# Kernel optimization log

Measured on AMD Instinct MI355X. Metric: run time of the kernel, lower is better.

Reference implementation:

```python
import jax, jax.numpy as jnp
import numpy as np
import math

HIDDEN = 2048
N_HEADS = 8
N_KV_HEADS = 1
HEAD_DIM = 256
ROPE_THETA = 10000.0
B, S = 1, 4096


def setup_inputs() -> dict:
    key = jax.random.key(0)
    ks = jax.random.split(key, 5)
    hidden_states = jax.random.normal(ks[0], (B, S, HIDDEN), dtype=jnp.float32)
    attention_mask = jnp.zeros((B, 1, S, S), dtype=jnp.float32)
    position_ids = jnp.arange(S, dtype=jnp.int64 if jax.config.jax_enable_x64 else jnp.int32)[None, :].repeat(B, axis=0)
    scale = 1.0 / math.sqrt(HIDDEN)
    Wq = jax.random.normal(ks[1], (HIDDEN, N_HEADS * HEAD_DIM), dtype=jnp.float32) * scale
    Wk = jax.random.normal(ks[2], (HIDDEN, N_KV_HEADS * HEAD_DIM), dtype=jnp.float32) * scale
    Wv = jax.random.normal(ks[3], (HIDDEN, N_KV_HEADS * HEAD_DIM), dtype=jnp.float32) * scale
    Wo = jax.random.normal(ks[4], (N_HEADS * HEAD_DIM, HIDDEN), dtype=jnp.float32) * scale
    return {"hidden_states": hidden_states, "attention_mask": attention_mask,
            "position_ids": position_ids, "Wq": Wq, "Wk": Wk, "Wv": Wv, "Wo": Wo}


def _rope_cos_sin(position_ids):
    # inv_freq: [HEAD_DIM/2]
    inv_freq = 1.0 / (ROPE_THETA ** (jnp.arange(0, HEAD_DIM, 2, dtype=jnp.float32) / HEAD_DIM))
    freqs = position_ids.astype(jnp.float32)[:, :, None] * inv_freq[None, None, :]  # [b,s,d/2]
    emb = jnp.concatenate([freqs, freqs], axis=-1)  # [b,s,d]
    return jnp.cos(emb), jnp.sin(emb)


def _rotate_half(x):
    x1, x2 = jnp.split(x, 2, axis=-1)
    return jnp.concatenate([-x2, x1], axis=-1)


def reference(hidden_states, attention_mask, position_ids, Wq, Wk, Wv, Wo):
    b, s, _ = hidden_states.shape
    g = N_HEADS // N_KV_HEADS  # kv groups
    # projections -> [b, heads, s, d]
    q = (hidden_states @ Wq).reshape(b, s, N_HEADS, HEAD_DIM).transpose(0, 2, 1, 3)
    k = (hidden_states @ Wk).reshape(b, s, N_KV_HEADS, HEAD_DIM).transpose(0, 2, 1, 3)
    v = (hidden_states @ Wv).reshape(b, s, N_KV_HEADS, HEAD_DIM).transpose(0, 2, 1, 3)
    # rotary embedding
    cos, sin = _rope_cos_sin(position_ids)  # [b,s,d]
    cos = cos[:, None, :, :]
    sin = sin[:, None, :, :]
    q = q * cos + _rotate_half(q) * sin
    k = k * cos + _rotate_half(k) * sin
    # GQA: group q heads against shared kv heads (no materialized repeat_kv)
    qg = q.reshape(b, N_KV_HEADS, g, s, HEAD_DIM)
    scores = jnp.einsum('bkgqd,bkld->bkgql', qg, k) / math.sqrt(HEAD_DIM)  # [b,kv,g,s,s]
    scores = scores.reshape(b, N_HEADS, s, s) + attention_mask
    attn = jax.nn.softmax(scores, axis=-1)
    out = jnp.einsum('bkgql,bkld->bkgqd', attn.reshape(b, N_KV_HEADS, g, s, s), v)
    out = out.reshape(b, N_HEADS, s, HEAD_DIM).transpose(0, 2, 1, 3).reshape(b, s, N_HEADS * HEAD_DIM)
    return out @ Wo
```

## Files before the change

kernel.cpp:

```cpp
#include <hip/hip_runtime.h>

typedef __bf16 bf16x8 __attribute__((ext_vector_type(8)));
typedef float f32x4 __attribute__((ext_vector_type(4)));
typedef float f32x16 __attribute__((ext_vector_type(16)));
typedef unsigned int u32x4 __attribute__((ext_vector_type(4)));
typedef unsigned short u16x4 __attribute__((ext_vector_type(4)));

__device__ __forceinline__ unsigned short f2bf(float f) {
  unsigned int u = __float_as_uint(f);
  u += 0x7FFF + ((u >> 16) & 1);
  return (unsigned short)(u >> 16);
}
__device__ __forceinline__ unsigned int packbf(float a, float b) {
  return (unsigned int)f2bf(a) | ((unsigned int)f2bf(b) << 16);
}
__device__ __forceinline__ void gl2lds16(const void* g, void* l) {
  __builtin_amdgcn_global_load_lds(
      (const __attribute__((address_space(1))) unsigned int*)(unsigned long long)g,
      (__attribute__((address_space(3))) unsigned int*)(unsigned long long)l,
      16, 0, 0);
}

__global__ void cvt_bf16_kernel(const float* __restrict__ in,
                                unsigned short* __restrict__ out, int n) {
  int i = (blockIdx.x * 256 + threadIdx.x) * 4;
  if (i >= n) return;
  float4 v = *(const float4*)&in[i];
  u16x4 o = { f2bf(v.x), f2bf(v.y), f2bf(v.z), f2bf(v.w) };
  *(u16x4*)&out[i] = o;
}

__global__ void transpose_cvt_kernel(const float* __restrict__ in,
                                     unsigned short* __restrict__ out, int R, int C) {
  __shared__ float t[32][33];
  int c0 = blockIdx.x * 32, r0 = blockIdx.y * 32;
  int tx = threadIdx.x & 31, ty = threadIdx.x >> 5;
#pragma unroll
  for (int i = 0; i < 4; i++)
    t[ty + i * 8][tx] = in[(size_t)(r0 + ty + i * 8) * C + c0 + tx];
  __syncthreads();
#pragma unroll
  for (int i = 0; i < 4; i++)
    out[(size_t)(c0 + ty + i * 8) * R + r0 + tx] = f2bf(t[tx][ty + i * 8]);
}

__global__ void rope_kernel(const float* __restrict__ Qf, const float* __restrict__ Kf,
                            const int* __restrict__ pos_ids,
                            unsigned short* __restrict__ Qb, unsigned short* __restrict__ Kimg) {
  int i = blockIdx.x * 256 + threadIdx.x;
  const int QN = 4096 * 1024;
  int s, d;
  float x1, x2;
  int h = 0;
  bool isQ = (i < QN);
  if (isQ) {
    s = i >> 10;
    int rem = i & 1023;
    h = rem >> 7;
    d = rem & 127;
    size_t b = (size_t)s * 2048 + h * 256 + d;
    x1 = Qf[b];
    x2 = Qf[b + 128];
  } else {
    int j = i - QN;
    if (j >= 4096 * 128) return;
    s = j >> 7;
    d = j & 127;
    x1 = Kf[(size_t)s * 256 + d];
    x2 = Kf[(size_t)s * 256 + d + 128];
  }
  int p = pos_ids[s];
  float invf = (float)exp2(-(double)d * (13.287712379549449 / 128.0));
  float th = (float)p * invf;
  double thd = (double)th;
  float c = (float)cos(thd), sn = (float)sin(thd);
  float o1 = x1 * c - x2 * sn;
  float o2 = x2 * c + x1 * sn;
  if (isQ) {
    size_t base = ((size_t)h * 4096 + s) * 256;
    Qb[base + d] = f2bf(o1 * 0.0625f);
    Qb[base + d + 128] = f2bf(o2 * 0.0625f);
  } else {
    int blk = s >> 5, kk = s & 31;
    size_t base = (size_t)blk * 8192 + kk * 256;
    int d1 = d, d2 = d + 128;
    Kimg[base + (((d1 >> 3) ^ (kk & 15)) * 8) + (d1 & 7)] = f2bf(o1);
    Kimg[base + (((d2 >> 3) ^ (kk & 15)) * 8) + (d2 & 7)] = f2bf(o2);
  }
}

__global__ void vimg_kernel(const float* __restrict__ Vf, unsigned short* __restrict__ Vimg) {
  __shared__ float t[32][257];
  int blk = blockIdx.x;
  int tid = threadIdx.x;
#pragma unroll
  for (int i = 0; i < 32; i++)
    t[i][tid] = Vf[((size_t)blk * 32 + i) * 256 + tid];
  __syncthreads();
  int d = tid;
  unsigned short* out = Vimg + (size_t)blk * 8192 + d * 32;
#pragma unroll
  for (int c = 0; c < 4; c++) {
    u16x4 a = { f2bf(t[c*8+0][d]), f2bf(t[c*8+1][d]), f2bf(t[c*8+2][d]), f2bf(t[c*8+3][d]) };
    u16x4 b = { f2bf(t[c*8+4][d]), f2bf(t[c*8+5][d]), f2bf(t[c*8+6][d]), f2bf(t[c*8+7][d]) };
    int cc = ((c ^ (d & 3)) * 8);
    *(u16x4*)&out[cc] = a;
    *(u16x4*)&out[cc + 4] = b;
  }
}

__global__ __launch_bounds__(256) void gemm_bt_kernel(
    const unsigned short* __restrict__ A, const unsigned short* __restrict__ BT,
    float* __restrict__ C0, float* __restrict__ C1, float* __restrict__ C2,
    int K, int mode) {
  __shared__ unsigned short As[128 * 32];
  __shared__ unsigned short Bs[128 * 32];
  int tid = threadIdx.x;
  int lane = tid & 63, w = tid >> 6;
  int quad = lane >> 4, l16 = lane & 15;
  int wr = w >> 1, wc = w & 1;
  int m0 = blockIdx.x * 128, n0 = blockIdx.y * 128;
  f32x4 acc[4][4] = {};

  for (int k0 = 0; k0 < K; k0 += 32) {
#pragma unroll
    for (int i = 0; i < 2; i++) {
      int idx = tid + i * 256;
      int row = idx >> 2, c = idx & 3;
      int sw = (c ^ (row & 3) ^ ((row >> 2) & 3)) * 8;
      *(u32x4*)&As[row * 32 + sw] = *(const u32x4*)&A[(size_t)(m0 + row) * K + k0 + c * 8];
      *(u32x4*)&Bs[row * 32 + sw] = *(const u32x4*)&BT[(size_t)(n0 + row) * K + k0 + c * 8];
    }
    __syncthreads();
    bf16x8 af[4], bfr[4];
#pragma unroll
    for (int mt = 0; mt < 4; mt++) {
      int r = wr * 64 + mt * 16 + l16;
      af[mt] = *(const bf16x8*)&As[r * 32 + ((quad ^ (r & 3) ^ ((r >> 2) & 3)) * 8)];
    }
#pragma unroll
    for (int nt = 0; nt < 4; nt++) {
      int r = wc * 64 + nt * 16 + l16;
      bfr[nt] = *(const bf16x8*)&Bs[r * 32 + ((quad ^ (r & 3) ^ ((r >> 2) & 3)) * 8)];
    }
#pragma unroll
    for (int mt = 0; mt < 4; mt++)
#pragma unroll
      for (int nt = 0; nt < 4; nt++)
        acc[mt][nt] = __builtin_amdgcn_mfma_f32_16x16x32_bf16(af[mt], bfr[nt], acc[mt][nt], 0, 0, 0);
    __syncthreads();
  }

  float* Cb;
  int ld, coff;
  if (mode == 0 || n0 < 2048) { Cb = C0; ld = 2048; coff = 0; }
  else if (n0 < 2304)         { Cb = C1; ld = 256;  coff = 2048; }
  else                        { Cb = C2; ld = 256;  coff = 2304; }
#pragma unroll
  for (int mt = 0; mt < 4; mt++) {
    int row = m0 + wr * 64 + mt * 16 + quad * 4;
#pragma unroll
    for (int nt = 0; nt < 4; nt++) {
      int col = n0 + wc * 64 + nt * 16 + l16 - coff;
#pragma unroll
      for (int r = 0; r < 4; r++)
        Cb[(size_t)(row + r) * ld + col] = acc[mt][nt][r];
    }
  }
}

__global__ __launch_bounds__(256, 1) void attn_kernel(
    const unsigned short* __restrict__ Qb, const unsigned short* __restrict__ Kimg,
    const unsigned short* __restrict__ Vimg, unsigned short* __restrict__ Ob) {
  __shared__ __align__(16) unsigned short smem[32768];
  const int tid = threadIdx.x;
  const int lane = tid & 63, w = tid >> 6;
  const int l32 = lane & 31, h = lane >> 5;
  const int head = blockIdx.y;
  const int q0 = blockIdx.x * 128 + w * 32;

  bf16x8 qb[16];
  {
    const unsigned short* qrow = Qb + ((size_t)head * 4096 + q0 + l32) * 256;
#pragma unroll
    for (int c = 0; c < 16; c++)
      qb[c] = *(const bf16x8*)&qrow[c * 16 + h * 8];
  }

  f32x16 acc[8] = {};
  float m_r = -3.0e38f, l_r = 0.0f;

  auto stage = [&](int blk, int slot) {
    const unsigned short* kg = Kimg + (size_t)blk * 8192 + w * 2048 + lane * 8;
    const unsigned short* vg = Vimg + (size_t)blk * 8192 + w * 2048 + lane * 8;
    unsigned short* kl = &smem[slot * 16384 + w * 2048];
    unsigned short* vl = &smem[slot * 16384 + 8192 + w * 2048];
#pragma unroll
    for (int i = 0; i < 4; i++) gl2lds16(kg + i * 512, kl + i * 512);
#pragma unroll
    for (int i = 0; i < 4; i++) gl2lds16(vg + i * 512, vl + i * 512);
  };

  int slot = 0;
  stage(0, 0);
  for (int blk = 0; blk < 128; blk++) {
    __syncthreads();
    if (blk + 1 < 128) stage(blk + 1, slot ^ 1);
    const unsigned short* Ks = &smem[slot * 16384];
    const unsigned short* Vs = &smem[slot * 16384 + 8192];

    f32x16 S = {};
#pragma unroll
    for (int c = 0; c < 16; c++) {
      bf16x8 kf = *(const bf16x8*)&Ks[l32 * 256 + (((2 * c + h) ^ (l32 & 15)) * 8)];
      S = __builtin_amdgcn_mfma_f32_32x32x16_bf16(kf, qb[c], S, 0, 0, 0);
    }

    float mx = S[0];
#pragma unroll
    for (int i = 1; i < 16; i++) mx = fmaxf(mx, S[i]);
    mx = fmaxf(mx, __shfl_xor(mx, 32));
    float mnew = fmaxf(m_r, mx);
    unsigned long long upd = __ballot(mnew > m_r);
    float alpha = __expf(m_r - mnew);
    m_r = mnew;
    float p[16];
    float rs = 0.0f;
#pragma unroll
    for (int i = 0; i < 16; i++) { p[i] = __expf(S[i] - mnew); rs += p[i]; }
    rs += __shfl_xor(rs, 32);
    l_r = l_r * alpha + rs;
    if (upd) {
#pragma unroll
      for (int dt = 0; dt < 8; dt++)
#pragma unroll
        for (int i = 0; i < 16; i++) acc[dt][i] *= alpha;
    }

    unsigned int pgx[4], pgy[4], qgx[4], qgy[4];
#pragma unroll
    for (int g = 0; g < 4; g++) {
      pgx[g] = packbf(p[4 * g + 0], p[4 * g + 1]);
      pgy[g] = packbf(p[4 * g + 2], p[4 * g + 3]);
      qgx[g] = (unsigned int)__shfl_xor((int)pgx[g], 32);
      qgy[g] = (unsigned int)__shfl_xor((int)pgy[g], 32);
    }

#pragma unroll
    for (int kc = 0; kc < 2; kc++) {
      union { unsigned int u[4]; bf16x8 v; } pf;
      pf.u[0] = h ? qgx[2 * kc + 1] : pgx[2 * kc];
      pf.u[1] = h ? qgy[2 * kc + 1] : pgy[2 * kc];
      pf.u[2] = h ? pgx[2 * kc + 1] : qgx[2 * kc];
      pf.u[3] = h ? pgy[2 * kc + 1] : qgy[2 * kc];
#pragma unroll
      for (int dt = 0; dt < 8; dt++) {
        bf16x8 vf = *(const bf16x8*)&Vs[(dt * 32 + l32) * 32 + (((kc * 2 + h) ^ (l32 & 3)) * 8)];
        acc[dt] = __builtin_amdgcn_mfma_f32_32x32x16_bf16(vf, pf.v, acc[dt], 0, 0, 0);
      }
    }
    slot ^= 1;
  }

  __syncthreads();
  unsigned short* lw = &smem[w * 8192];
  float linv = 1.0f / l_r;
#pragma unroll
  for (int dt = 0; dt < 8; dt++) {
#pragma unroll
    for (int g = 0; g < 4; g++) {
      int d0 = dt * 32 + 8 * g + 4 * h;
      uint2 pk;
      pk.x = packbf(acc[dt][4 * g + 0] * linv, acc[dt][4 * g + 1] * linv);
      pk.y = packbf(acc[dt][4 * g + 2] * linv, acc[dt][4 * g + 3] * linv);
      *(uint2*)&lw[l32 * 256 + d0] = pk;
    }
  }
  const size_t obase = (size_t)q0 * 2048 + head * 256;
#pragma unroll
  for (int i = 0; i < 16; i++) {
    int row = i * 2 + h;
    u32x4 vv = *(const u32x4*)&lw[row * 256 + l32 * 8];
    *(u32x4*)&Ob[obase + (size_t)row * 2048 + l32 * 8] = vv;
  }
}

extern "C" void kernel_launch(void* const* d_in, const int* in_sizes, int n_in,
                              void* d_out, int out_size, void* d_ws, size_t ws_size,
                              hipStream_t stream) {
  const float* X  = (const float*)d_in[0];
  const int* pos  = (const int*)d_in[2];
  const float* Wq = (const float*)d_in[3];
  const float* Wk = (const float*)d_in[4];
  const float* Wv = (const float*)d_in[5];
  const float* Wo = (const float*)d_in[6];
  float* Y = (float*)d_out;
  char* ws = (char*)d_ws;

  unsigned short* WoT  = (unsigned short*)(ws + 0);
  unsigned short* Xb   = (unsigned short*)(ws + 8388608);
  unsigned short* Wqkv = (unsigned short*)(ws + 25165824);
  float* Qf = (float*)(ws + 35651584);
  float* Kf = (float*)(ws + 69206016);
  float* Vf = (float*)(ws + 73400320);
  unsigned short* Qbb  = (unsigned short*)(ws + 8388608);
  unsigned short* Kimg = (unsigned short*)(ws + 25165824);
  unsigned short* Vimg = (unsigned short*)(ws + 27262976);
  unsigned short* Obb  = (unsigned short*)(ws + 35651584);

  cvt_bf16_kernel<<<8192, 256, 0, stream>>>(X, Xb, 4096 * 2048);
  transpose_cvt_kernel<<<dim3(64, 64), 256, 0, stream>>>(Wq, Wqkv, 2048, 2048);
  transpose_cvt_kernel<<<dim3(8, 64), 256, 0, stream>>>(Wk, Wqkv + 2048 * 2048, 2048, 256);
  transpose_cvt_kernel<<<dim3(8, 64), 256, 0, stream>>>(Wv, Wqkv + 2048 * 2048 + 256 * 2048, 2048, 256);
  transpose_cvt_kernel<<<dim3(64, 64), 256, 0, stream>>>(Wo, WoT, 2048, 2048);

  gemm_bt_kernel<<<dim3(32, 20), 256, 0, stream>>>(Xb, Wqkv, Qf, Kf, Vf, 2048, 1);

  rope_kernel<<<18432, 256, 0, stream>>>(Qf, Kf, pos, Qbb, Kimg);
  vimg_kernel<<<128, 256, 0, stream>>>(Vf, Vimg);

  attn_kernel<<<dim3(32, 8), 256, 0, stream>>>(Qbb, Kimg, Vimg, Obb);

  gemm_bt_kernel<<<dim3(32, 16), 256, 0, stream>>>(Obb, WoT, Y, nullptr, nullptr, 2048, 0);
}
```

Measured before the change: 579.8 us.

## Split attention over KV halves with merge, async LDS loads in GEMM

Attention is split along the key dimension into two halves (split-K flash attention). This doubles the grid from 256 to 512 blocks so the CUs stay busier, and launch bounds now allow two blocks per CU. A new merge kernel combines the partial outputs using the saved max and sum statistics. The QK product uses two independent accumulators to cut the MFMA dependency chain, and the V image swizzle is changed to reduce LDS bank conflicts. The GEMM now loads tiles with global_load_lds instead of going through registers, at the cost of extra partial-output traffic and one more kernel launch.

Measured after the change: 489.4 us. 15.6% less time.

```diff
diff --git a/kernel.cpp b/kernel.cpp
--- a/kernel.cpp
+++ b/kernel.cpp
@@ -13,6 +13,9 @@
 }
 __device__ __forceinline__ unsigned int packbf(float a, float b) {
   return (unsigned int)f2bf(a) | ((unsigned int)f2bf(b) << 16);
+}
+__device__ __forceinline__ float bf2f(unsigned short s) {
+  return __uint_as_float(((unsigned int)s) << 16);
 }
 __device__ __forceinline__ void gl2lds16(const void* g, void* l) {
   __builtin_amdgcn_global_load_lds(
@@ -103,7 +106,7 @@
   for (int c = 0; c < 4; c++) {
     u16x4 a = { f2bf(t[c*8+0][d]), f2bf(t[c*8+1][d]), f2bf(t[c*8+2][d]), f2bf(t[c*8+3][d]) };
     u16x4 b = { f2bf(t[c*8+4][d]), f2bf(t[c*8+5][d]), f2bf(t[c*8+6][d]), f2bf(t[c*8+7][d]) };
-    int cc = ((c ^ (d & 3)) * 8);
+    int cc = ((c ^ ((d >> 1) & 3)) * 8);
     *(u16x4*)&out[cc] = a;
     *(u16x4*)&out[cc + 4] = b;
   }
@@ -113,8 +116,8 @@
     const unsigned short* __restrict__ A, const unsigned short* __restrict__ BT,
     float* __restrict__ C0, float* __restrict__ C1, float* __restrict__ C2,
     int K, int mode) {
-  __shared__ unsigned short As[128 * 32];
-  __shared__ unsigned short Bs[128 * 32];
+  __shared__ __align__(16) unsigned short As[128 * 32];
+  __shared__ __align__(16) unsigned short Bs[128 * 32];
   int tid = threadIdx.x;
   int lane = tid & 63, w = tid >> 6;
   int quad = lane >> 4, l16 = lane & 15;
@@ -122,15 +125,26 @@
   int m0 = blockIdx.x * 128, n0 = blockIdx.y * 128;
   f32x4 acc[4][4] = {};
 
+  const unsigned short *ga0, *ga1, *gb0, *gb1;
+  unsigned short *la0, *la1, *lb0, *lb1;
+  {
+    int j0 = tid, j1 = tid + 256;
+    int r0 = j0 >> 2, c0 = (j0 & 3) ^ (r0 & 3) ^ ((r0 >> 2) & 3);
+    int r1 = j1 >> 2, c1 = (j1 & 3) ^ (r1 & 3) ^ ((r1 >> 2) & 3);
+    ga0 = A + (size_t)(m0 + r0) * K + c0 * 8;
+    ga1 = A + (size_t)(m0 + r1) * K + c1 * 8;
+    gb0 = BT + (size_t)(n0 + r0) * K + c0 * 8;
+    gb1 = BT + (size_t)(n0 + r1) * K + c1 * 8;
+    la0 = As + (size_t)(w * 64) * 8;
+    la1 = As + (size_t)(256 + w * 64) * 8;
+    lb0 = Bs + (size_t)(w * 64) * 8;
+    lb1 = Bs + (size_t)(256 + w * 64) * 8;
+  }
+
   for (int k0 = 0; k0 < K; k0 += 32) {
-#pragma unroll
-    for (int i = 0; i < 2; i++) {
-      int idx = tid + i * 256;
-      int row = idx >> 2, c = idx & 3;
-      int sw = (c ^ (row & 3) ^ ((row >> 2) & 3)) * 8;
-      *(u32x4*)&As[row * 32 + sw] = *(const u32x4*)&A[(size_t)(m0 + row) * K + k0 + c * 8];
-      *(u32x4*)&Bs[row * 32 + sw] = *(const u32x4*)&BT[(size_t)(n0 + row) * K + k0 + c * 8];
-    }
+    gl2lds16(ga0, la0); gl2lds16(ga1, la1);
+    gl2lds16(gb0, lb0); gl2lds16(gb1, lb1);
+    ga0 += 32; ga1 += 32; gb0 += 32; gb1 += 32;
     __syncthreads();
     bf16x8 af[4], bfr[4];
 #pragma unroll
@@ -169,14 +183,16 @@
   }
 }
 
-__global__ __launch_bounds__(256, 1) void attn_kernel(
+__global__ __launch_bounds__(256, 2) void attn_kernel(
     const unsigned short* __restrict__ Qb, const unsigned short* __restrict__ Kimg,
-    const unsigned short* __restrict__ Vimg, unsigned short* __restrict__ Ob) {
+    const unsigned short* __restrict__ Vimg, unsigned short* __restrict__ Opart,
+    float2* __restrict__ ML) {
   __shared__ __align__(16) unsigned short smem[32768];
   const int tid = threadIdx.x;
   const int lane = tid & 63, w = tid >> 6;
   const int l32 = lane & 31, h = lane >> 5;
   const int head = blockIdx.y;
+  const int half = blockIdx.z;
   const int q0 = blockIdx.x * 128 + w * 32;
 
   bf16x8 qb[16];
@@ -201,20 +217,24 @@
     for (int i = 0; i < 4; i++) gl2lds16(vg + i * 512, vl + i * 512);
   };
 
+  const int blk0 = half * 64, blk_end = blk0 + 64;
   int slot = 0;
-  stage(0, 0);
-  for (int blk = 0; blk < 128; blk++) {
+  stage(blk0, 0);
+  for (int blk = blk0; blk < blk_end; blk++) {
     __syncthreads();
-    if (blk + 1 < 128) stage(blk + 1, slot ^ 1);
+    if (blk + 1 < blk_end) stage(blk + 1, slot ^ 1);
     const unsigned short* Ks = &smem[slot * 16384];
     const unsigned short* Vs = &smem[slot * 16384 + 8192];
 
-    f32x16 S = {};
-#pragma unroll
-    for (int c = 0; c < 16; c++) {
-      bf16x8 kf = *(const bf16x8*)&Ks[l32 * 256 + (((2 * c + h) ^ (l32 & 15)) * 8)];
-      S = __builtin_amdgcn_mfma_f32_32x32x16_bf16(kf, qb[c], S, 0, 0, 0);
-    }
+    f32x16 Sa = {}, Sb = {};
+#pragma unroll
+    for (int c = 0; c < 8; c++) {
+      bf16x8 kf0 = *(const bf16x8*)&Ks[l32 * 256 + (((2 * c + h) ^ (l32 & 15)) * 8)];
+      bf16x8 kf1 = *(const bf16x8*)&Ks[l32 * 256 + (((2 * (c + 8) + h) ^ (l32 & 15)) * 8)];
+      Sa = __builtin_amdgcn_mfma_f32_32x32x16_bf16(kf0, qb[c], Sa, 0, 0, 0);
+      Sb = __builtin_amdgcn_mfma_f32_32x32x16_bf16(kf1, qb[c + 8], Sb, 0, 0, 0);
+    }
+    f32x16 S = Sa + Sb;
 
     float mx = S[0];
 #pragma unroll
@@ -255,7 +275,7 @@
       pf.u[3] = h ? pgy[2 * kc + 1] : qgy[2 * kc];
 #pragma unroll
       for (int dt = 0; dt < 8; dt++) {
-        bf16x8 vf = *(const bf16x8*)&Vs[(dt * 32 + l32) * 32 + (((kc * 2 + h) ^ (l32 & 3)) * 8)];
+        bf16x8 vf = *(const bf16x8*)&Vs[(dt * 32 + l32) * 32 + (((kc * 2 + h) ^ ((l32 >> 1) & 3)) * 8)];
         acc[dt] = __builtin_amdgcn_mfma_f32_32x32x16_bf16(vf, pf.v, acc[dt], 0, 0, 0);
       }
     }
@@ -276,13 +296,45 @@
       *(uint2*)&lw[l32 * 256 + d0] = pk;
     }
   }
-  const size_t obase = (size_t)q0 * 2048 + head * 256;
+  const size_t obase = ((size_t)(half * 8 + head) * 4096 + q0) * 256;
 #pragma unroll
   for (int i = 0; i < 16; i++) {
     int row = i * 2 + h;
     u32x4 vv = *(const u32x4*)&lw[row * 256 + l32 * 8];
-    *(u32x4*)&Ob[obase + (size_t)row * 2048 + l32 * 8] = vv;
-  }
+    *(u32x4*)&Opart[obase + (size_t)row * 256 + l32 * 8] = vv;
+  }
+  if (h == 0)
+    ML[((size_t)half * 8 + head) * 4096 + q0 + l32] = make_float2(m_r, l_r);
+}
+
+__global__ void merge_kernel(const unsigned short* __restrict__ Opart,
+                             const float2* __restrict__ ML,
+                             unsigned short* __restrict__ Obb) {
+  int idx = blockIdx.x * 256 + threadIdx.x;
+  int dc = idx & 31;
+  int q = (idx >> 5) & 4095;
+  int head = idx >> 17;
+  float2 a = ML[(size_t)head * 4096 + q];
+  float2 b = ML[(size_t)(8 + head) * 4096 + q];
+  float m = fmaxf(a.x, b.x);
+  float c0 = __expf(a.x - m) * a.y;
+  float c1 = __expf(b.x - m) * b.y;
+  float inv = 1.0f / (c0 + c1);
+  c0 *= inv; c1 *= inv;
+  size_t o0 = ((size_t)head * 4096 + q) * 256 + dc * 8;
+  u16x4 p0a = *(const u16x4*)&Opart[o0];
+  u16x4 p0b = *(const u16x4*)&Opart[o0 + 4];
+  u16x4 p1a = *(const u16x4*)&Opart[o0 + 8u * 4096u * 256u];
+  u16x4 p1b = *(const u16x4*)&Opart[o0 + 8u * 4096u * 256u + 4];
+  u16x4 ra, rb;
+#pragma unroll
+  for (int i = 0; i < 4; i++) {
+    ra[i] = f2bf(c0 * bf2f(p0a[i]) + c1 * bf2f(p1a[i]));
+    rb[i] = f2bf(c0 * bf2f(p0b[i]) + c1 * bf2f(p1b[i]));
+  }
+  unsigned short* out = &Obb[(size_t)q * 2048 + head * 256 + dc * 8];
+  *(u16x4*)out = ra;
+  *(u16x4*)(out + 4) = rb;
 }
 
 extern "C" void kernel_launch(void* const* d_in, const int* in_sizes, int n_in,
@@ -303,10 +355,12 @@
   float* Qf = (float*)(ws + 35651584);
   float* Kf = (float*)(ws + 69206016);
   float* Vf = (float*)(ws + 73400320);
-  unsigned short* Qbb  = (unsigned short*)(ws + 8388608);
-  unsigned short* Kimg = (unsigned short*)(ws + 25165824);
-  unsigned short* Vimg = (unsigned short*)(ws + 27262976);
-  unsigned short* Obb  = (unsigned short*)(ws + 35651584);
+  unsigned short* Qbb   = (unsigned short*)(ws + 8388608);
+  unsigned short* Kimg  = (unsigned short*)(ws + 25165824);
+  unsigned short* Vimg  = (unsigned short*)(ws + 27262976);
+  unsigned short* Opart = (unsigned short*)(ws + 35651584);
+  float2* ML            = (float2*)(ws + 69206016);
+  unsigned short* Obb   = (unsigned short*)(ws + 8388608);
 
   cvt_bf16_kernel<<<8192, 256, 0, stream>>>(X, Xb, 4096 * 2048);
   transpose_cvt_kernel<<<dim3(64, 64), 256, 0, stream>>>(Wq, Wqkv, 2048, 2048);
@@ -319,7 +373,8 @@
   rope_kernel<<<18432, 256, 0, stream>>>(Qf, Kf, pos, Qbb, Kimg);
   vimg_kernel<<<128, 256, 0, stream>>>(Vf, Vimg);
 
-  attn_kernel<<<dim3(32, 8), 256, 0, stream>>>(Qbb, Kimg, Vimg, Obb);
+  attn_kernel<<<dim3(32, 8, 2), 256, 0, stream>>>(Qbb, Kimg, Vimg, Opart, ML);
+  merge_kernel<<<4096, 256, 0, stream>>>(Opart, ML, Obb);
 
   gemm_bt_kernel<<<dim3(32, 16), 256, 0, stream>>>(Obb, WoT, Y, nullptr, nullptr, 2048, 0);
 }
```
